# Optimization experiments

Hardware: AMD Instinct MI355X
Metric: run time of the kernel (lower is better)

The kernel has to match this reference:

```python
import jax, jax.numpy as jnp
import numpy as np
import math

B, T = 2, 1024
D_MODEL = 1024
N_HEAD = 16
HEAD_DIM = D_MODEL // N_HEAD
VOCAB = 32000
NUM_LOOP = 4
EPS_LN = 1e-5                       # torch LayerNorm default
EPS_RMS = float(np.finfo(np.float32).eps)  # torch RMSNorm eps=None -> finfo eps


def setup_inputs() -> dict:
    key = jax.random.key(0)
    ks = jax.random.split(key, 12)
    s = 0.02
    d = D_MODEL
    tok = jax.random.normal(ks[1], (VOCAB, d), jnp.float32) * s
    tok = tok.at[0].set(0.0)  # padding_idx=0
    return {
        "idx": jax.random.randint(ks[0], (B, T), 0, VOCAB),
        "tok_embed": tok,
        "ln_e_g": jnp.ones((d,), jnp.float32),
        "ln_e_b": jnp.zeros((d,), jnp.float32),
        "Wqkv": jax.random.normal(ks[2], (d, 3 * d), jnp.float32) * s,
        "bqkv": jnp.zeros((3 * d,), jnp.float32),
        "Wo": jax.random.normal(ks[3], (d, d), jnp.float32) * s,
        "bo": jnp.zeros((d,), jnp.float32),
        "W1": jax.random.normal(ks[4], (d, 4 * d), jnp.float32) * s,
        "b1": jnp.zeros((4 * d,), jnp.float32),
        "W2": jax.random.normal(ks[5], (4 * d, d), jnp.float32) * s,
        "b2": jnp.zeros((d,), jnp.float32),
        "n1_w": jnp.ones((d,), jnp.float32),
        "n2_w": jnp.ones((d,), jnp.float32),
        "lnf_g": jnp.ones((d,), jnp.float32),
        "lnf_b": jnp.zeros((d,), jnp.float32),
        "Wlm": jax.random.normal(ks[6], (d, VOCAB), jnp.float32) * s,
        "blm": jnp.zeros((VOCAB,), jnp.float32),
    }


def layernorm(x, g, b):
    m = jnp.mean(x, axis=-1, keepdims=True)
    v = jnp.mean(jnp.square(x - m), axis=-1, keepdims=True)
    return (x - m) * jax.lax.rsqrt(v + EPS_LN) * g + b


def rmsnorm(x, w):
    ms = jnp.mean(jnp.square(x), axis=-1, keepdims=True)
    return x * jax.lax.rsqrt(ms + EPS_RMS) * w


def gelu_tanh(x):
    c = math.sqrt(2.0 / math.pi)
    return 0.5 * x * (1.0 + jnp.tanh(c * (x + 0.044715 * x * x * x)))


def alibi_causal_bias(t):
    # rpe[q,k] = -(q-k) for q>k else 0, scaled per head by 2^(-8/H*(h+1)); causal -inf above diag
    pos = jnp.arange(t)
    rel = pos[:, None] - pos[None, :]                      # [T,T] = q - k
    slopes = 2.0 ** (-8.0 / N_HEAD * jnp.arange(1, N_HEAD + 1, dtype=jnp.float32))
    bias = -slopes[:, None, None] * rel.astype(jnp.float32)  # [H,T,T]
    return jnp.where(rel[None] >= 0, bias, -jnp.inf)       # causal mask fused


def reference(idx, tok_embed, ln_e_g, ln_e_b, Wqkv, bqkv, Wo, bo,
              W1, b1, W2, b2, n1_w, n2_w, lnf_g, lnf_b, Wlm, blm):
    b, t = idx.shape
    x = layernorm(tok_embed[idx], ln_e_g, ln_e_b)          # rpe=True: no sinusoidal PE
    bias = alibi_causal_bias(t)                            # [H,T,T]
    scale = 1.0 / math.sqrt(HEAD_DIM)

    for _ in range(NUM_LOOP):
        # attention sublayer
        h = rmsnorm(x, n1_w)
        qkv = h @ Wqkv + bqkv
        q, k, v = jnp.split(qkv, 3, axis=-1)
        q = q.reshape(b, t, N_HEAD, HEAD_DIM).transpose(0, 2, 1, 3)
        k = k.reshape(b, t, N_HEAD, HEAD_DIM).transpose(0, 2, 1, 3)
        v = v.reshape(b, t, N_HEAD, HEAD_DIM).transpose(0, 2, 1, 3)
        att = jnp.einsum('bhqd,bhkd->bhqk', q, k) * scale + bias[None]
        att = jax.nn.softmax(att, axis=-1)
        y = jnp.einsum('bhqk,bhkd->bhqd', att, v)
        y = y.transpose(0, 2, 1, 3).reshape(b, t, D_MODEL)
        x = x + (y @ Wo + bo)
        # mlp sublayer
        h = rmsnorm(x, n2_w)
        x = x + (gelu_tanh(h @ W1 + b1) @ W2 + b2)

    x = layernorm(x, lnf_g, lnf_b)
    return x @ Wlm + blm  # [B,T,VOCAB]
```

## Files before the change

### kernel.cpp

```cpp
#include <hip/hip_runtime.h>
#include <stdint.h>

#define DEVI __device__ __forceinline__

typedef __attribute__((ext_vector_type(8))) short short8;
typedef __attribute__((ext_vector_type(4))) float f32x4;
typedef unsigned short u16;
typedef unsigned int u32;

typedef const __attribute__((address_space(1))) void* gas_ptr;
typedef __attribute__((address_space(3))) void* las_ptr;

constexpr int BBATCH = 2;
constexpr int TT  = 1024;
constexpr int BT  = BBATCH * TT;
constexpr int DM  = 1024;
constexpr int NH  = 16;
constexpr int HD  = 64;
constexpr int DFF = 4096;
constexpr int NV  = 32000;
constexpr int NL  = 4;

DEVI u16 f2b(float f) {
  u32 u = __builtin_bit_cast(u32, f);
  u = (u + 0x7fffu + ((u >> 16) & 1u)) >> 16;
  return (u16)u;
}
DEVI float b2f(u16 h) { return __builtin_bit_cast(float, (u32)h << 16); }

DEVI void gld16(const void* g, void* l) {
  __builtin_amdgcn_global_load_lds((gas_ptr)g, (las_ptr)l, 16, 0, 0);
}

DEVI float wave_sum(float v) {
#pragma unroll
  for (int off = 32; off; off >>= 1) v += __shfl_xor(v, off);
  return v;
}
DEVI float block_sum(float v, float* sb) {
  v = wave_sum(v);
  int lane = threadIdx.x & 63, wid = threadIdx.x >> 6;
  __syncthreads();
  if (lane == 0) sb[wid] = v;
  __syncthreads();
  return sb[0] + sb[1] + sb[2] + sb[3];
}

DEVI float gelu_f(float x) {
  float u = 0.7978845608028654f * (x + 0.044715f * x * x * x);
  float e = __expf(2.0f * u);
  return x * (1.0f - 1.0f / (e + 1.0f));
}

__global__ __launch_bounds__(256) void wt_transpose_all(
    const float* __restrict__ Wqkv, const float* __restrict__ Wo,
    const float* __restrict__ W1, const float* __restrict__ W2,
    const float* __restrict__ Wlm,
    u16* __restrict__ WqkvT, u16* __restrict__ WoT, u16* __restrict__ W1T,
    u16* __restrict__ W2T, u16* __restrict__ WlmT) {
  __shared__ float t[32][33];
  int bid = blockIdx.x;
  const float* in; u16* out; int K, N, tt;
  if (bid < 3072)       { in = Wqkv; out = WqkvT; K = 1024; N = 3072;  tt = bid; }
  else if (bid < 4096)  { in = Wo;   out = WoT;   K = 1024; N = 1024;  tt = bid - 3072; }
  else if (bid < 8192)  { in = W1;   out = W1T;   K = 1024; N = 4096;  tt = bid - 4096; }
  else if (bid < 12288) { in = W2;   out = W2T;   K = 4096; N = 1024;  tt = bid - 8192; }
  else                  { in = Wlm;  out = WlmT;  K = 1024; N = 32000; tt = bid - 12288; }
  int nx = N >> 5;
  int n0 = (tt % nx) * 32, k0 = (tt / nx) * 32;
  int tx = threadIdx.x & 31, ty = threadIdx.x >> 5;
#pragma unroll
  for (int i = 0; i < 4; ++i)
    t[ty + 8 * i][tx] = in[(size_t)(k0 + ty + 8 * i) * N + n0 + tx];
  __syncthreads();
#pragma unroll
  for (int i = 0; i < 4; ++i)
    out[(size_t)(n0 + ty + 8 * i) * K + k0 + tx] = f2b(t[tx][ty + 8 * i]);
}

__global__ __launch_bounds__(256) void embed_ln_k(const int* __restrict__ idx,
                                                  const float* __restrict__ tok,
                                                  const float* __restrict__ g,
                                                  const float* __restrict__ b,
                                                  float* __restrict__ x) {
  __shared__ float sb[4];
  int row = blockIdx.x, tid = threadIdx.x;
  float4 v = ((const float4*)(tok + (size_t)idx[row] * DM))[tid];
  float s = block_sum(v.x + v.y + v.z + v.w, sb);
  float m = s * (1.0f / DM);
  float dx = v.x - m, dy = v.y - m, dz = v.z - m, dw = v.w - m;
  float q = block_sum(dx * dx + dy * dy + dz * dz + dw * dw, sb);
  float rs = rsqrtf(q * (1.0f / DM) + 1e-5f);
  float4 gg = ((const float4*)g)[tid];
  float4 bb = ((const float4*)b)[tid];
  float4 o = make_float4(dx * rs * gg.x + bb.x, dy * rs * gg.y + bb.y,
                         dz * rs * gg.z + bb.z, dw * rs * gg.w + bb.w);
  ((float4*)(x + (size_t)row * DM))[tid] = o;
}

__global__ __launch_bounds__(256) void final_ln_k(const float* __restrict__ x,
                                                  const float* __restrict__ g,
                                                  const float* __restrict__ b,
                                                  u16* __restrict__ xf) {
  __shared__ float sb[4];
  int row = blockIdx.x, tid = threadIdx.x;
  float4 v = ((const float4*)(x + (size_t)row * DM))[tid];
  float s = block_sum(v.x + v.y + v.z + v.w, sb);
  float m = s * (1.0f / DM);
  float dx = v.x - m, dy = v.y - m, dz = v.z - m, dw = v.w - m;
  float q = block_sum(dx * dx + dy * dy + dz * dz + dw * dw, sb);
  float rs = rsqrtf(q * (1.0f / DM) + 1e-5f);
  float4 gg = ((const float4*)g)[tid];
  float4 bb = ((const float4*)b)[tid];
  u32 lo = (u32)f2b(dx * rs * gg.x + bb.x) | ((u32)f2b(dy * rs * gg.y + bb.y) << 16);
  u32 hi = (u32)f2b(dz * rs * gg.z + bb.z) | ((u32)f2b(dw * rs * gg.w + bb.w) << 16);
  ((uint2*)(xf + (size_t)row * DM))[tid] = make_uint2(lo, hi);
}

__global__ __launch_bounds__(256) void rmsnorm_k(const float* __restrict__ x,
                                                 const float* __restrict__ w,
                                                 u16* __restrict__ h) {
  __shared__ float sb[4];
  int row = blockIdx.x, tid = threadIdx.x;
  float4 v = ((const float4*)(x + (size_t)row * DM))[tid];
  float q = block_sum(v.x * v.x + v.y * v.y + v.z * v.z + v.w * v.w, sb);
  float rs = rsqrtf(q * (1.0f / DM) + 1.1920928955078125e-7f);
  float4 ww = ((const float4*)w)[tid];
  u32 lo = (u32)f2b(v.x * rs * ww.x) | ((u32)f2b(v.y * rs * ww.y) << 16);
  u32 hi = (u32)f2b(v.z * rs * ww.z) | ((u32)f2b(v.w * rs * ww.w) << 16);
  ((uint2*)(h + (size_t)row * DM))[tid] = make_uint2(lo, hi);
}

__global__ __launch_bounds__(256) void attn_k(const u16* __restrict__ qkv,
                                              const u16* __restrict__ vT,
                                              u16* __restrict__ y) {
  __shared__ __align__(16) char sP[32768];
  __shared__ __align__(16) char sK[2][16384];
  __shared__ __align__(16) char sV[2][16384];
  const int tid = threadIdx.x, lane = tid & 63, wid = tid >> 6;
  const int qt = blockIdx.x, bh = blockIdx.y, b = bh >> 4, h = bh & 15;
  const float slope = exp2f(-0.5f * (float)(h + 1));

  const char* Qb = (const char*)(qkv + (size_t)b * TT * 3 * DM + h * HD);
  const char* Kb = (const char*)(qkv + (size_t)b * TT * 3 * DM + DM + h * HD);
  const char* Vb = (const char*)(vT + (size_t)bh * HD * TT);

#pragma unroll
  for (int ci = 0; ci < 4; ++ci) {
    int c = wid * 4 + ci;
    int r = c * 8 + (lane >> 3);
    int q = (lane & 7) ^ (r & 7);
    gld16(Qb + (size_t)(qt * 128 + r) * 6144 + q * 16, sP + c * 1024 + lane * 16);
  }

  auto stageKV = [&](int buf, int kt) {
    int kv0 = kt * 128;
#pragma unroll
    for (int ci = 0; ci < 4; ++ci) {
      int c = wid * 4 + ci;
      int r = c * 8 + (lane >> 3);
      int q = (lane & 7) ^ (r & 7);
      gld16(Kb + (size_t)(kv0 + r) * 6144 + q * 16, sK[buf] + c * 1024 + lane * 16);
    }
#pragma unroll
    for (int ci = 0; ci < 4; ++ci) {
      int c = wid * 4 + ci;
      int d = c * 4 + (lane >> 4);
      int q = (lane & 15) ^ (d & 15);
      gld16(Vb + (size_t)d * 2048 + (size_t)kv0 * 2 + q * 16, sV[buf] + c * 1024 + lane * 16);
    }
  };
  stageKV(0, 0);
  asm volatile("s_waitcnt vmcnt(8)" ::: "memory");

  short8 qf[2][2];
#pragma unroll
  for (int i = 0; i < 2; ++i)
#pragma unroll
    for (int ks = 0; ks < 2; ++ks) {
      int r = wid * 32 + i * 16 + (lane & 15);
      int q = ((ks << 2) + (lane >> 4)) ^ (r & 7);
      qf[i][ks] = *(const short8*)(sP + r * 128 + q * 16);
    }

  f32x4 Y[2][4] = {};
  float m_r[2][4], l_r[2][4];
#pragma unroll
  for (int i = 0; i < 2; ++i)
#pragma unroll
    for (int r = 0; r < 4; ++r) { m_r[i][r] = -3e38f; l_r[i][r] = 0.0f; }

  for (int kt = 0; kt <= qt; ++kt) {
    const int cur = kt & 1;
    if (kt < qt) {
      stageKV(cur ^ 1, kt + 1);
      asm volatile("s_waitcnt vmcnt(8)" ::: "memory");
    } else {
      asm volatile("s_waitcnt vmcnt(0)" ::: "memory");
    }
    __syncthreads();

    f32x4 s[2][8] = {};
    __builtin_amdgcn_s_setprio(1);
#pragma unroll
    for (int ks = 0; ks < 2; ++ks) {
      short8 kf[8];
#pragma unroll
      for (int j = 0; j < 8; ++j) {
        int r = j * 16 + (lane & 15);
        int q = ((ks << 2) + (lane >> 4)) ^ (r & 7);
        kf[j] = *(const short8*)(sK[cur] + r * 128 + q * 16);
      }
#pragma unroll
      for (int i = 0; i < 2; ++i)
#pragma unroll
        for (int j = 0; j < 8; ++j)
          s[i][j] = __builtin_amdgcn_mfma_f32_16x16x32_bf16(qf[i][ks], kf[j], s[i][j], 0, 0, 0);
    }
    __builtin_amdgcn_s_setprio(0);

    const int kv0 = kt * 128;
#pragma unroll
    for (int i = 0; i < 2; ++i) {
      const int qbase = qt * 128 + wid * 32 + i * 16 + ((lane >> 4) << 2);
      float rowmax[4] = {-3e38f, -3e38f, -3e38f, -3e38f};
#pragma unroll
      for (int j = 0; j < 8; ++j) {
        int kcol = kv0 + j * 16 + (lane & 15);
#pragma unroll
        for (int r = 0; r < 4; ++r) {
          int qrow = qbase + r;
          float v = (kcol <= qrow) ? s[i][j][r] * 0.125f - slope * (float)(qrow - kcol) : -3e38f;
          s[i][j][r] = v;
          rowmax[r] = fmaxf(rowmax[r], v);
        }
      }
#pragma unroll
      for (int r = 0; r < 4; ++r) {
        rowmax[r] = fmaxf(rowmax[r], __shfl_xor(rowmax[r], 1));
        rowmax[r] = fmaxf(rowmax[r], __shfl_xor(rowmax[r], 2));
        rowmax[r] = fmaxf(rowmax[r], __shfl_xor(rowmax[r], 4));
        rowmax[r] = fmaxf(rowmax[r], __shfl_xor(rowmax[r], 8));
        float mn = fmaxf(m_r[i][r], rowmax[r]);
        float al = __expf(m_r[i][r] - mn);
        m_r[i][r] = mn;
        l_r[i][r] *= al;
#pragma unroll
        for (int j = 0; j < 4; ++j) Y[i][j][r] *= al;
      }
      float rs[4] = {0.0f, 0.0f, 0.0f, 0.0f};
#pragma unroll
      for (int j = 0; j < 8; ++j)
#pragma unroll
        for (int r = 0; r < 4; ++r) {
          float p = __expf(s[i][j][r] - m_r[i][r]);
          s[i][j][r] = p;
          rs[r] += p;
        }
#pragma unroll
      for (int r = 0; r < 4; ++r) {
        rs[r] += __shfl_xor(rs[r], 1);
        rs[r] += __shfl_xor(rs[r], 2);
        rs[r] += __shfl_xor(rs[r], 4);
        rs[r] += __shfl_xor(rs[r], 8);
        l_r[i][r] += rs[r];
      }
#pragma unroll
      for (int j = 0; j < 8; ++j)
#pragma unroll
        for (int r = 0; r < 4; ++r) {
          int rl = wid * 32 + i * 16 + ((lane >> 4) << 2) + r;
          int c = j * 16 + (lane & 15);
          int g = c >> 3;
          *(u16*)(sP + rl * 256 + ((g ^ (rl & 15)) << 4) + (c & 7) * 2) = f2b(s[i][j][r]);
        }
    }

    __builtin_amdgcn_s_setprio(1);
#pragma unroll
    for (int ks = 0; ks < 4; ++ks) {
      short8 pf[2], vf[4];
#pragma unroll
      for (int i = 0; i < 2; ++i) {
        int r = wid * 32 + i * 16 + (lane & 15);
        int q = ((ks << 2) + (lane >> 4)) ^ (r & 15);
        pf[i] = *(const short8*)(sP + r * 256 + (q << 4));
      }
#pragma unroll
      for (int j = 0; j < 4; ++j) {
        int d = j * 16 + (lane & 15);
        int q = ((ks << 2) + (lane >> 4)) ^ (d & 15);
        vf[j] = *(const short8*)(sV[cur] + d * 256 + (q << 4));
      }
#pragma unroll
      for (int i = 0; i < 2; ++i)
#pragma unroll
        for (int j = 0; j < 4; ++j)
          Y[i][j] = __builtin_amdgcn_mfma_f32_16x16x32_bf16(pf[i], vf[j], Y[i][j], 0, 0, 0);
    }
    __builtin_amdgcn_s_setprio(0);
    __syncthreads();
  }

#pragma unroll
  for (int i = 0; i < 2; ++i)
#pragma unroll
    for (int r = 0; r < 4; ++r) {
      float inv = 1.0f / l_r[i][r];
      int qrow = qt * 128 + wid * 32 + i * 16 + ((lane >> 4) << 2) + r;
      u16* yp = y + (size_t)(b * TT + qrow) * DM + h * HD;
#pragma unroll
      for (int j = 0; j < 4; ++j)
        yp[j * 16 + (lane & 15)] = f2b(Y[i][j][r] * inv);
    }
}

enum { EPI_BF16 = 0, EPI_GELU = 1, EPI_ADDF32 = 2, EPI_F32 = 3, EPI_ATOMIC = 4, EPI_QKV = 5 };

template <int BM, int BN, int WM, int WN, int EPI, int KS = 1>
__global__ __launch_bounds__(256, 2) void gemm_bt(
    const u16* __restrict__ A, int lda, const u16* __restrict__ Bt, int ldb,
    const float* __restrict__ bias, void* __restrict__ C, int ldc,
    float* __restrict__ resid, int K, u16* __restrict__ vTout) {
  constexpr int BK = 64;
  constexpr int NW = WM * WN;
  constexpr int FM = BM / WM / 16, FN = BN / WN / 16;
  constexpr int ABYTES = BM * BK * 2, BBYTES = BN * BK * 2;
  constexpr int ACH = ABYTES / 1024, BCH = BBYTES / 1024, NCH = ACH + BCH;
  extern __shared__ __align__(16) char smem[];

  const int tid = threadIdx.x, lane = tid & 63, wid = tid >> 6;
  const int brow = blockIdx.y * BM, bcol = blockIdx.x * BN;
  const long long kbase2 = (long long)blockIdx.z * (K / KS) * 2;

  const int nt = (K / KS) >> 6;
  const int widm = wid / WN, widn = wid % WN;
  const int rm0 = widm * (BM / WM), cn0 = widn * (BN / WN);

  f32x4 acc[FM][FN] = {};

  const int swq16 = (((lane & 7) ^ ((lane >> 3) & 7)) << 4);
  const int lrow8 = lane >> 3;

  auto stage = [&](int buf, int kt) {
    char* base = smem + buf * (ABYTES + BBYTES);
    const char* Ag = (const char*)A;
    const char* Bg = (const char*)Bt;
    long long kOff = kbase2 + (long long)kt * 128 + swq16;
#pragma unroll
    for (int ci = 0; ci < NCH / NW; ++ci) {
      int c = wid + ci * NW;
      if (c < ACH) {
        int r = c * 8 + lrow8;
        gld16(Ag + (long long)(brow + r) * (lda * 2) + kOff, base + c * 1024 + lane * 16);
      } else {
        int r = (c - ACH) * 8 + lrow8;
        gld16(Bg + (long long)(bcol + r) * (ldb * 2) + kOff,
              base + ABYTES + (c - ACH) * 1024 + lane * 16);
      }
    }
  };

  auto compute = [&](int buf) {
    char* baseA = smem + buf * (ABYTES + BBYTES);
    char* baseB = baseA + ABYTES;
#pragma unroll
    for (int ks = 0; ks < 2; ++ks) {
      short8 af[FM], bv[FN];
#pragma unroll
      for (int i = 0; i < FM; ++i) {
        int r = rm0 + i * 16 + (lane & 15);
        int cq = ((ks << 2) + (lane >> 4)) ^ (r & 7);
        af[i] = *(const short8*)(baseA + r * 128 + (cq << 4));
      }
#pragma unroll
      for (int j = 0; j < FN; ++j) {
        int r = cn0 + j * 16 + (lane & 15);
        int cq = ((ks << 2) + (lane >> 4)) ^ (r & 7);
        bv[j] = *(const short8*)(baseB + r * 128 + (cq << 4));
      }
#pragma unroll
      for (int i = 0; i < FM; ++i)
#pragma unroll
        for (int j = 0; j < FN; ++j)
          acc[i][j] = __builtin_amdgcn_mfma_f32_16x16x32_bf16(af[i], bv[j], acc[i][j], 0, 0, 0);
    }
  };

  stage(0, 0);
  __syncthreads();
  int cur = 0;
  for (int t = 0; t < nt; ++t) {
    if (t + 1 < nt) stage(cur ^ 1, t + 1);
    compute(cur);
    __syncthreads();
    cur ^= 1;
  }

  if constexpr (EPI == EPI_QKV) {
    if (bcol >= 2 * DM) {
      u16* st = (u16*)smem;
#pragma unroll
      for (int i = 0; i < FM; ++i)
#pragma unroll
        for (int j = 0; j < FN; ++j)
#pragma unroll
          for (int r = 0; r < 4; ++r) {
            int rl = rm0 + i * 16 + ((lane >> 4) << 2) + r;
            int cl = cn0 + j * 16 + (lane & 15);
            st[rl * 130 + cl] = f2b(acc[i][j][r] + bias[bcol + cl]);
          }
      __syncthreads();
      const int b = brow >> 10, t0b = brow & (TT - 1);
      const int h0 = (bcol - 2 * DM) >> 6;
      const int sub = tid & 15;
#pragma unroll
      for (int pass = 0; pass < 8; ++pass) {
        int d = pass * 16 + (tid >> 4);
        u32 pk[4];
#pragma unroll
        for (int k2 = 0; k2 < 4; ++k2) {
          u16 lo = st[(sub * 8 + 2 * k2) * 130 + d];
          u16 hi = st[(sub * 8 + 2 * k2 + 1) * 130 + d];
          pk[k2] = (u32)lo | ((u32)hi << 16);
        }
        int head = h0 + (d >> 6), dd = d & 63;
        *(uint4*)(vTout + ((size_t)((b * NH + head) * HD + dd)) * TT + t0b + sub * 8) =
            make_uint4(pk[0], pk[1], pk[2], pk[3]);
      }
      return;
    }
  }

  const int r0 = brow + rm0 + ((lane >> 4) << 2);
  const int c0 = bcol + cn0 + (lane & 15);
#pragma unroll
  for (int i = 0; i < FM; ++i) {
#pragma unroll
    for (int j = 0; j < FN; ++j) {
#pragma unroll
      for (int r = 0; r < 4; ++r) {
        int row = r0 + i * 16 + r;
        int col = c0 + j * 16;
        float v = acc[i][j][r];
        if constexpr (EPI == EPI_BF16 || EPI == EPI_QKV) {
          ((u16*)C)[(size_t)row * ldc + col] = f2b(v + bias[col]);
        } else if constexpr (EPI == EPI_GELU) {
          ((u16*)C)[(size_t)row * ldc + col] = f2b(gelu_f(v + bias[col]));
        } else if constexpr (EPI == EPI_ADDF32) {
          size_t o = (size_t)row * ldc + col;
          resid[o] += v + bias[col];
        } else if constexpr (EPI == EPI_ATOMIC) {
          size_t o = (size_t)row * ldc + col;
          atomicAdd(&resid[o], v + (blockIdx.z == 0 ? bias[col] : 0.0f));
        } else {
          ((float*)C)[(size_t)row * ldc + col] = v + bias[col];
        }
      }
    }
  }
}

template <int EPI>
__global__ __launch_bounds__(512, 2) void gemm8(
    const u16* __restrict__ A, int lda, const u16* __restrict__ Bt, int ldb,
    const float* __restrict__ bias, void* __restrict__ C, int ldc, int K, int nby) {
  __shared__ __align__(16) char smem[2][2][32768];
  const int tid = threadIdx.x, lane = tid & 63;
  const int wid = tid >> 6, wm = wid >> 2, wn = wid & 3;

  const int nb = gridDim.x;
  const int q8 = nb >> 3, r8 = nb & 7;
  const int xcd = blockIdx.x & 7, lin = blockIdx.x >> 3;
  const int idx = (xcd < r8 ? xcd * (q8 + 1) : r8 * (q8 + 1) + (xcd - r8) * q8) + lin;
  const int brow = (idx % nby) * 256, bcol = (idx / nby) * 256;

  const int nt = K >> 6, niter = nt >> 1;

  const int srow = tid >> 3, sq = tid & 7;
  auto stage = [&](int buf, int isB, int half, int kt) {
    const u16* G = isB ? Bt : A;
    const int ld = isB ? ldb : lda;
    const int base = isB ? bcol : brow;
    char* L = &smem[buf][isB][half * 16384];
#pragma unroll
    for (int l = 0; l < 2; ++l) {
      int rl = half * 128 + l * 64 + srow;
      gld16((const char*)G + (size_t)(base + rl) * (ld * 2) + kt * 128 + ((sq ^ (rl & 7)) << 4),
            L + l * 8192 + tid * 16);
    }
  };

  short8 bfr[4][2], afr[2][2];
  f32x4 acc[8][4] = {};

  stage(0, 0, 0, 0); stage(0, 0, 1, 0);
  stage(0, 1, 0, 0); stage(0, 1, 1, 0);
  stage(1, 1, 0, 1); stage(1, 1, 1, 1);
  asm volatile("s_waitcnt vmcnt(0)" ::: "memory");
  __builtin_amdgcn_s_barrier();

  for (int i = 0; i < niter; ++i) {
    const bool full = (i + 1 < niter);
    const int t2 = 2 * i + 2, t3 = 2 * i + 3;
#pragma unroll
    for (int h = 0; h < 2; ++h) {
#pragma unroll
      for (int qd = 0; qd < 4; ++qd) {
        if (qd == 0) {
#pragma unroll
          for (int j = 0; j < 4; ++j)
#pragma unroll
            for (int ks = 0; ks < 2; ++ks) {
              int r = wn * 64 + j * 16 + (lane & 15);
              int q = ((ks << 2) + (lane >> 4)) ^ (r & 7);
              bfr[j][ks] = *(const short8*)&smem[h][1][r * 128 + q * 16];
            }
        }
#pragma unroll
        for (int f = 0; f < 2; ++f)
#pragma unroll
          for (int ks = 0; ks < 2; ++ks) {
            int r = wm * 128 + (qd * 2 + f) * 16 + (lane & 15);
            int q = ((ks << 2) + (lane >> 4)) ^ (r & 7);
            afr[f][ks] = *(const short8*)&smem[h][0][r * 128 + q * 16];
          }
        if (h == 0) {
          if (qd == 0) stage(1, 0, 0, 2 * i + 1);
          else if (qd == 1) stage(1, 0, 1, 2 * i + 1);
          else if (qd == 2) { if (full) stage(0, 1, 0, t2); }
          else              { if (full) stage(0, 1, 1, t2); }
        } else {
          if (qd == 0)      { if (full) stage(0, 0, 0, t2); }
          else if (qd == 1) { if (full) stage(0, 0, 1, t2); }
          else if (qd == 2) { if (full) stage(1, 1, 0, t3); }
          else              { if (full) stage(1, 1, 1, t3); }
        }
        if (qd == 3) {
          if (full) asm volatile("s_waitcnt vmcnt(4)" ::: "memory");
          else if (h == 0) asm volatile("s_waitcnt vmcnt(0)" ::: "memory");
        }
        __builtin_amdgcn_s_barrier();
        asm volatile("s_waitcnt lgkmcnt(0)" ::: "memory");
        __builtin_amdgcn_s_setprio(1);
#pragma unroll
        for (int f = 0; f < 2; ++f)
#pragma unroll
          for (int j = 0; j < 4; ++j)
#pragma unroll
            for (int ks = 0; ks < 2; ++ks)
              acc[qd * 2 + f][j] = __builtin_amdgcn_mfma_f32_16x16x32_bf16(
                  afr[f][ks], bfr[j][ks], acc[qd * 2 + f][j], 0, 0, 0);
        __builtin_amdgcn_s_setprio(0);
        __builtin_amdgcn_s_barrier();
      }
    }
  }

  const int r0 = brow + wm * 128 + ((lane >> 4) << 2);
  const int c0 = bcol + wn * 64 + (lane & 15);
#pragma unroll
  for (int fi = 0; fi < 8; ++fi) {
#pragma unroll
    for (int j = 0; j < 4; ++j) {
      int col = c0 + j * 16;
      float bv = bias[col];
#pragma unroll
      for (int r = 0; r < 4; ++r) {
        int row = r0 + fi * 16 + r;
        float v = acc[fi][j][r] + bv;
        if constexpr (EPI == EPI_F32)
          ((float*)C)[(size_t)row * ldc + col] = v;
        else if constexpr (EPI == EPI_GELU)
          ((u16*)C)[(size_t)row * ldc + col] = f2b(gelu_f(v));
        else
          ((u16*)C)[(size_t)row * ldc + col] = f2b(v);
      }
    }
  }
}

extern "C" void kernel_launch(void* const* d_in, const int* in_sizes, int n_in,
                              void* d_out, int out_size, void* d_ws, size_t ws_size,
                              hipStream_t stream) {
  (void)in_sizes; (void)n_in; (void)out_size;
  const int*   idx    = (const int*)d_in[0];
  const float* tok    = (const float*)d_in[1];
  const float* ln_e_g = (const float*)d_in[2];
  const float* ln_e_b = (const float*)d_in[3];
  const float* Wqkv   = (const float*)d_in[4];
  const float* bqkv   = (const float*)d_in[5];
  const float* Wo     = (const float*)d_in[6];
  const float* bo     = (const float*)d_in[7];
  const float* W1     = (const float*)d_in[8];
  const float* b1     = (const float*)d_in[9];
  const float* W2     = (const float*)d_in[10];
  const float* b2     = (const float*)d_in[11];
  const float* n1_w   = (const float*)d_in[12];
  const float* n2_w   = (const float*)d_in[13];
  const float* lnf_g  = (const float*)d_in[14];
  const float* lnf_b  = (const float*)d_in[15];
  const float* Wlm    = (const float*)d_in[16];
  const float* blm    = (const float*)d_in[17];
  float* out = (float*)d_out;

  char* w = (char*)d_ws;
  auto alloc = [&](size_t bytes) { char* p = w; w += (bytes + 255) & ~(size_t)255; return p; };
  float* x   = (float*)alloc((size_t)BT * DM * 4);
  u16* h     = (u16*)alloc((size_t)BT * DM * 2);
  u16* qkv   = (u16*)alloc((size_t)BT * 3 * DM * 2);
  u16* vT    = (u16*)alloc((size_t)BBATCH * NH * HD * TT * 2);
  u16* y     = (u16*)alloc((size_t)BT * DM * 2);
  u16* act   = (u16*)alloc((size_t)BT * DFF * 2);
  u16* xf    = (u16*)alloc((size_t)BT * DM * 2);
  u16* WqkvT = (u16*)alloc((size_t)3 * DM * DM * 2);
  u16* WoT   = (u16*)alloc((size_t)DM * DM * 2);
  u16* W1T   = (u16*)alloc((size_t)DFF * DM * 2);
  u16* W2T   = (u16*)alloc((size_t)DM * DFF * 2);
  u16* WlmT  = (u16*)alloc((size_t)NV * DM * 2);
  if ((size_t)(w - (char*)d_ws) > ws_size) return;

  wt_transpose_all<<<44288, 256, 0, stream>>>(Wqkv, Wo, W1, W2, Wlm,
                                              WqkvT, WoT, W1T, W2T, WlmT);

  embed_ln_k<<<BT, 256, 0, stream>>>(idx, tok, ln_e_g, ln_e_b, x);

  constexpr int SM128 = 2 * (128 * 64 * 2 + 128 * 64 * 2);
  constexpr int SM64  = 2 * (128 * 64 * 2 + 64 * 64 * 2);

  for (int l = 0; l < NL; ++l) {
    rmsnorm_k<<<BT, 256, 0, stream>>>(x, n1_w, h);
    gemm_bt<128, 128, 2, 2, EPI_QKV><<<dim3(3 * DM / 128, BT / 128), 256, SM128, stream>>>(
        h, DM, WqkvT, DM, bqkv, qkv, 3 * DM, nullptr, DM, vT);
    attn_k<<<dim3(TT / 128, BBATCH * NH), 256, 0, stream>>>(qkv, vT, y);
    gemm_bt<128, 64, 4, 1, EPI_ATOMIC, 2><<<dim3(DM / 64, BT / 128, 2), 256, SM64, stream>>>(
        y, DM, WoT, DM, bo, nullptr, DM, x, DM, nullptr);
    rmsnorm_k<<<BT, 256, 0, stream>>>(x, n2_w, h);
    gemm_bt<128, 128, 2, 2, EPI_GELU><<<dim3(DFF / 128, BT / 128), 256, SM128, stream>>>(
        h, DM, W1T, DM, b1, act, DFF, nullptr, DM, nullptr);
    gemm_bt<128, 128, 2, 2, EPI_ATOMIC, 4><<<dim3(DM / 128, BT / 128, 4), 256, SM128, stream>>>(
        act, DFF, W2T, DFF, b2, nullptr, DM, x, DFF, nullptr);
  }

  final_ln_k<<<BT, 256, 0, stream>>>(x, lnf_g, lnf_b, xf);
  gemm8<EPI_F32><<<dim3((NV / 256) * (BT / 256)), 512, 0, stream>>>(
      xf, DM, WlmT, DM, blm, out, NV, DM, BT / 256);
}
```

Before: 906.0 us.

## Split attention into 64-row query tiles with balanced ordering; stage LM-head stores via LDS

Attention now processes 64-row query tiles over a flat 512-block grid. Block indices are remapped so that long and short causal tiles interleave, and the KV double buffer is dropped to cut LDS use and raise occupancy. The fp32 LM-head GEMM epilogue writes its accumulators through swizzled shared memory and then emits coalesced float4 row stores. The trade-off is losing the KV load/compute overlap in attention and adding extra barriers in the epilogue.

Measured after the change: 851.5 us. -6.0%, faster.

```diff
diff --git a/kernel.cpp b/kernel.cpp
--- a/kernel.cpp
+++ b/kernel.cpp
@@ -134,11 +134,15 @@
 __global__ __launch_bounds__(256) void attn_k(const u16* __restrict__ qkv,
                                               const u16* __restrict__ vT,
                                               u16* __restrict__ y) {
-  __shared__ __align__(16) char sP[32768];
-  __shared__ __align__(16) char sK[2][16384];
-  __shared__ __align__(16) char sV[2][16384];
+  __shared__ __align__(16) char sP[16384];
+  __shared__ __align__(16) char sK[16384];
+  __shared__ __align__(16) char sV[16384];
   const int tid = threadIdx.x, lane = tid & 63, wid = tid >> 6;
-  const int qt = blockIdx.x, bh = blockIdx.y, b = bh >> 4, h = bh & 15;
+  const int bid = blockIdx.x;
+  const int sl = (bid + (bid >> 8)) & 15;
+  const int qt = (sl & 1) ? (sl >> 1) : (15 - (sl >> 1));
+  const int bh = (bid >> 4) & 31, b = bh >> 4, h = bh & 15;
+  const int nt = (qt >> 1) + 1;
   const float slope = exp2f(-0.5f * (float)(h + 1));
 
   const char* Qb = (const char*)(qkv + (size_t)b * TT * 3 * DM + h * HD);
@@ -146,61 +150,51 @@
   const char* Vb = (const char*)(vT + (size_t)bh * HD * TT);
 
 #pragma unroll
-  for (int ci = 0; ci < 4; ++ci) {
-    int c = wid * 4 + ci;
+  for (int ci = 0; ci < 2; ++ci) {
+    int c = wid * 2 + ci;
     int r = c * 8 + (lane >> 3);
     int q = (lane & 7) ^ (r & 7);
-    gld16(Qb + (size_t)(qt * 128 + r) * 6144 + q * 16, sP + c * 1024 + lane * 16);
-  }
-
-  auto stageKV = [&](int buf, int kt) {
+    gld16(Qb + (size_t)(qt * 64 + r) * 6144 + q * 16, sP + c * 1024 + lane * 16);
+  }
+
+  auto stageKV = [&](int kt) {
     int kv0 = kt * 128;
 #pragma unroll
     for (int ci = 0; ci < 4; ++ci) {
       int c = wid * 4 + ci;
       int r = c * 8 + (lane >> 3);
       int q = (lane & 7) ^ (r & 7);
-      gld16(Kb + (size_t)(kv0 + r) * 6144 + q * 16, sK[buf] + c * 1024 + lane * 16);
+      gld16(Kb + (size_t)(kv0 + r) * 6144 + q * 16, sK + c * 1024 + lane * 16);
     }
 #pragma unroll
     for (int ci = 0; ci < 4; ++ci) {
       int c = wid * 4 + ci;
       int d = c * 4 + (lane >> 4);
       int q = (lane & 15) ^ (d & 15);
-      gld16(Vb + (size_t)d * 2048 + (size_t)kv0 * 2 + q * 16, sV[buf] + c * 1024 + lane * 16);
+      gld16(Vb + (size_t)d * 2048 + (size_t)kv0 * 2 + q * 16, sV + c * 1024 + lane * 16);
     }
   };
-  stageKV(0, 0);
+  stageKV(0);
   asm volatile("s_waitcnt vmcnt(8)" ::: "memory");
 
-  short8 qf[2][2];
-#pragma unroll
-  for (int i = 0; i < 2; ++i)
-#pragma unroll
-    for (int ks = 0; ks < 2; ++ks) {
-      int r = wid * 32 + i * 16 + (lane & 15);
-      int q = ((ks << 2) + (lane >> 4)) ^ (r & 7);
-      qf[i][ks] = *(const short8*)(sP + r * 128 + q * 16);
-    }
-
-  f32x4 Y[2][4] = {};
-  float m_r[2][4], l_r[2][4];
-#pragma unroll
-  for (int i = 0; i < 2; ++i)
-#pragma unroll
-    for (int r = 0; r < 4; ++r) { m_r[i][r] = -3e38f; l_r[i][r] = 0.0f; }
-
-  for (int kt = 0; kt <= qt; ++kt) {
-    const int cur = kt & 1;
-    if (kt < qt) {
-      stageKV(cur ^ 1, kt + 1);
-      asm volatile("s_waitcnt vmcnt(8)" ::: "memory");
-    } else {
-      asm volatile("s_waitcnt vmcnt(0)" ::: "memory");
-    }
+  short8 qf[2];
+#pragma unroll
+  for (int ks = 0; ks < 2; ++ks) {
+    int r = wid * 16 + (lane & 15);
+    int q = ((ks << 2) + (lane >> 4)) ^ (r & 7);
+    qf[ks] = *(const short8*)(sP + r * 128 + q * 16);
+  }
+
+  f32x4 Y[4] = {};
+  float m_r[4], l_r[4];
+#pragma unroll
+  for (int r = 0; r < 4; ++r) { m_r[r] = -3e38f; l_r[r] = 0.0f; }
+
+  for (int kt = 0; kt < nt; ++kt) {
+    asm volatile("s_waitcnt vmcnt(0)" ::: "memory");
     __syncthreads();
 
-    f32x4 s[2][8] = {};
+    f32x4 s[8] = {};
     __builtin_amdgcn_s_setprio(1);
 #pragma unroll
     for (int ks = 0; ks < 2; ++ks) {
@@ -209,110 +203,101 @@
       for (int j = 0; j < 8; ++j) {
         int r = j * 16 + (lane & 15);
         int q = ((ks << 2) + (lane >> 4)) ^ (r & 7);
-        kf[j] = *(const short8*)(sK[cur] + r * 128 + q * 16);
-      }
-#pragma unroll
-      for (int i = 0; i < 2; ++i)
-#pragma unroll
-        for (int j = 0; j < 8; ++j)
-          s[i][j] = __builtin_amdgcn_mfma_f32_16x16x32_bf16(qf[i][ks], kf[j], s[i][j], 0, 0, 0);
+        kf[j] = *(const short8*)(sK + r * 128 + q * 16);
+      }
+#pragma unroll
+      for (int j = 0; j < 8; ++j)
+        s[j] = __builtin_amdgcn_mfma_f32_16x16x32_bf16(qf[ks], kf[j], s[j], 0, 0, 0);
     }
     __builtin_amdgcn_s_setprio(0);
 
     const int kv0 = kt * 128;
-#pragma unroll
-    for (int i = 0; i < 2; ++i) {
-      const int qbase = qt * 128 + wid * 32 + i * 16 + ((lane >> 4) << 2);
-      float rowmax[4] = {-3e38f, -3e38f, -3e38f, -3e38f};
-#pragma unroll
-      for (int j = 0; j < 8; ++j) {
-        int kcol = kv0 + j * 16 + (lane & 15);
-#pragma unroll
-        for (int r = 0; r < 4; ++r) {
-          int qrow = qbase + r;
-          float v = (kcol <= qrow) ? s[i][j][r] * 0.125f - slope * (float)(qrow - kcol) : -3e38f;
-          s[i][j][r] = v;
-          rowmax[r] = fmaxf(rowmax[r], v);
-        }
-      }
+    const int qbase = qt * 64 + wid * 16 + ((lane >> 4) << 2);
+    float rowmax[4] = {-3e38f, -3e38f, -3e38f, -3e38f};
+#pragma unroll
+    for (int j = 0; j < 8; ++j) {
+      int kcol = kv0 + j * 16 + (lane & 15);
 #pragma unroll
       for (int r = 0; r < 4; ++r) {
-        rowmax[r] = fmaxf(rowmax[r], __shfl_xor(rowmax[r], 1));
-        rowmax[r] = fmaxf(rowmax[r], __shfl_xor(rowmax[r], 2));
-        rowmax[r] = fmaxf(rowmax[r], __shfl_xor(rowmax[r], 4));
-        rowmax[r] = fmaxf(rowmax[r], __shfl_xor(rowmax[r], 8));
-        float mn = fmaxf(m_r[i][r], rowmax[r]);
-        float al = __expf(m_r[i][r] - mn);
-        m_r[i][r] = mn;
-        l_r[i][r] *= al;
-#pragma unroll
-        for (int j = 0; j < 4; ++j) Y[i][j][r] *= al;
-      }
-      float rs[4] = {0.0f, 0.0f, 0.0f, 0.0f};
-#pragma unroll
-      for (int j = 0; j < 8; ++j)
-#pragma unroll
-        for (int r = 0; r < 4; ++r) {
-          float p = __expf(s[i][j][r] - m_r[i][r]);
-          s[i][j][r] = p;
-          rs[r] += p;
-        }
+        int qrow = qbase + r;
+        float v = (kcol <= qrow) ? s[j][r] * 0.125f - slope * (float)(qrow - kcol) : -3e38f;
+        s[j][r] = v;
+        rowmax[r] = fmaxf(rowmax[r], v);
+      }
+    }
+#pragma unroll
+    for (int r = 0; r < 4; ++r) {
+      rowmax[r] = fmaxf(rowmax[r], __shfl_xor(rowmax[r], 1));
+      rowmax[r] = fmaxf(rowmax[r], __shfl_xor(rowmax[r], 2));
+      rowmax[r] = fmaxf(rowmax[r], __shfl_xor(rowmax[r], 4));
+      rowmax[r] = fmaxf(rowmax[r], __shfl_xor(rowmax[r], 8));
+      float mn = fmaxf(m_r[r], rowmax[r]);
+      float al = __expf(m_r[r] - mn);
+      m_r[r] = mn;
+      l_r[r] *= al;
+#pragma unroll
+      for (int j = 0; j < 4; ++j) Y[j][r] *= al;
+    }
+    float rs[4] = {0.0f, 0.0f, 0.0f, 0.0f};
+#pragma unroll
+    for (int j = 0; j < 8; ++j)
 #pragma unroll
       for (int r = 0; r < 4; ++r) {
-        rs[r] += __shfl_xor(rs[r], 1);
-        rs[r] += __shfl_xor(rs[r], 2);
-        rs[r] += __shfl_xor(rs[r], 4);
-        rs[r] += __shfl_xor(rs[r], 8);
-        l_r[i][r] += rs[r];
-      }
-#pragma unroll
-      for (int j = 0; j < 8; ++j)
-#pragma unroll
-        for (int r = 0; r < 4; ++r) {
-          int rl = wid * 32 + i * 16 + ((lane >> 4) << 2) + r;
-          int c = j * 16 + (lane & 15);
-          int g = c >> 3;
-          *(u16*)(sP + rl * 256 + ((g ^ (rl & 15)) << 4) + (c & 7) * 2) = f2b(s[i][j][r]);
-        }
-    }
+        float p = __expf(s[j][r] - m_r[r]);
+        s[j][r] = p;
+        rs[r] += p;
+      }
+#pragma unroll
+    for (int r = 0; r < 4; ++r) {
+      rs[r] += __shfl_xor(rs[r], 1);
+      rs[r] += __shfl_xor(rs[r], 2);
+      rs[r] += __shfl_xor(rs[r], 4);
+      rs[r] += __shfl_xor(rs[r], 8);
+      l_r[r] += rs[r];
+    }
+#pragma unroll
+    for (int j = 0; j < 8; ++j)
+#pragma unroll
+      for (int r = 0; r < 4; ++r) {
+        int rl = wid * 16 + ((lane >> 4) << 2) + r;
+        int c = j * 16 + (lane & 15);
+        int g = c >> 3;
+        *(u16*)(sP + rl * 256 + ((g ^ (rl & 15)) << 4) + (c & 7) * 2) = f2b(s[j][r]);
+      }
 
     __builtin_amdgcn_s_setprio(1);
 #pragma unroll
     for (int ks = 0; ks < 4; ++ks) {
-      short8 pf[2], vf[4];
-#pragma unroll
-      for (int i = 0; i < 2; ++i) {
-        int r = wid * 32 + i * 16 + (lane & 15);
+      short8 pf, vf[4];
+      {
+        int r = wid * 16 + (lane & 15);
         int q = ((ks << 2) + (lane >> 4)) ^ (r & 15);
-        pf[i] = *(const short8*)(sP + r * 256 + (q << 4));
+        pf = *(const short8*)(sP + r * 256 + (q << 4));
       }
 #pragma unroll
       for (int j = 0; j < 4; ++j) {
         int d = j * 16 + (lane & 15);
         int q = ((ks << 2) + (lane >> 4)) ^ (d & 15);
-        vf[j] = *(const short8*)(sV[cur] + d * 256 + (q << 4));
-      }
-#pragma unroll
-      for (int i = 0; i < 2; ++i)
-#pragma unroll
-        for (int j = 0; j < 4; ++j)
-          Y[i][j] = __builtin_amdgcn_mfma_f32_16x16x32_bf16(pf[i], vf[j], Y[i][j], 0, 0, 0);
+        vf[j] = *(const short8*)(sV + d * 256 + (q << 4));
+      }
+#pragma unroll
+      for (int j = 0; j < 4; ++j)
+        Y[j] = __builtin_amdgcn_mfma_f32_16x16x32_bf16(pf, vf[j], Y[j], 0, 0, 0);
     }
     __builtin_amdgcn_s_setprio(0);
     __syncthreads();
-  }
-
-#pragma unroll
-  for (int i = 0; i < 2; ++i)
-#pragma unroll
-    for (int r = 0; r < 4; ++r) {
-      float inv = 1.0f / l_r[i][r];
-      int qrow = qt * 128 + wid * 32 + i * 16 + ((lane >> 4) << 2) + r;
-      u16* yp = y + (size_t)(b * TT + qrow) * DM + h * HD;
-#pragma unroll
-      for (int j = 0; j < 4; ++j)
-        yp[j * 16 + (lane & 15)] = f2b(Y[i][j][r] * inv);
-    }
+    if (kt + 1 < nt) stageKV(kt + 1);
+  }
+
+#pragma unroll
+  for (int r = 0; r < 4; ++r) {
+    float inv = 1.0f / l_r[r];
+    int qrow = qt * 64 + wid * 16 + ((lane >> 4) << 2) + r;
+    u16* yp = y + (size_t)(b * TT + qrow) * DM + h * HD;
+#pragma unroll
+    for (int j = 0; j < 4; ++j)
+      yp[j * 16 + (lane & 15)] = f2b(Y[j][r] * inv);
+  }
 }
 
 enum { EPI_BF16 = 0, EPI_GELU = 1, EPI_ADDF32 = 2, EPI_F32 = 3, EPI_ATOMIC = 4, EPI_QKV = 5 };
@@ -557,6 +542,39 @@
     }
   }
 
+  if constexpr (EPI == EPI_F32) {
+    char* sf = &smem[0][0][0];
+    float* C32 = (float*)C;
+#pragma unroll
+    for (int half = 0; half < 2; ++half) {
+      if (wm == half) {
+#pragma unroll
+        for (int fi = 0; fi < 8; ++fi)
+#pragma unroll
+          for (int j = 0; j < 4; ++j) {
+            int cl = wn * 64 + j * 16 + (lane & 15);
+            float bv = bias[bcol + cl];
+            int qsw = (cl >> 2);
+#pragma unroll
+            for (int r = 0; r < 4; ++r) {
+              int row = fi * 16 + ((lane >> 4) << 2) + r;
+              *(float*)(sf + row * 1024 + ((qsw ^ (row & 7)) << 4) + (cl & 3) * 4) =
+                  acc[fi][j][r] + bv;
+            }
+          }
+      }
+      __syncthreads();
+#pragma unroll
+      for (int pass = 0; pass < 16; ++pass) {
+        int row = pass * 8 + wid;
+        float4 v4 = *(float4*)(sf + row * 1024 + ((lane ^ (row & 7)) << 4));
+        *(float4*)(C32 + (size_t)(brow + half * 128 + row) * ldc + bcol + lane * 4) = v4;
+      }
+      __syncthreads();
+    }
+    return;
+  }
+
   const int r0 = brow + wm * 128 + ((lane >> 4) << 2);
   const int c0 = bcol + wn * 64 + (lane & 15);
 #pragma unroll
@@ -569,9 +587,7 @@
       for (int r = 0; r < 4; ++r) {
         int row = r0 + fi * 16 + r;
         float v = acc[fi][j][r] + bv;
-        if constexpr (EPI == EPI_F32)
-          ((float*)C)[(size_t)row * ldc + col] = v;
-        else if constexpr (EPI == EPI_GELU)
+        if constexpr (EPI == EPI_GELU)
           ((u16*)C)[(size_t)row * ldc + col] = f2b(gelu_f(v));
         else
           ((u16*)C)[(size_t)row * ldc + col] = f2b(v);
@@ -632,7 +648,7 @@
     rmsnorm_k<<<BT, 256, 0, stream>>>(x, n1_w, h);
     gemm_bt<128, 128, 2, 2, EPI_QKV><<<dim3(3 * DM / 128, BT / 128), 256, SM128, stream>>>(
         h, DM, WqkvT, DM, bqkv, qkv, 3 * DM, nullptr, DM, vT);
-    attn_k<<<dim3(TT / 128, BBATCH * NH), 256, 0, stream>>>(qkv, vT, y);
+    attn_k<<<512, 256, 0, stream>>>(qkv, vT, y);
     gemm_bt<128, 64, 4, 1, EPI_ATOMIC, 2><<<dim3(DM / 64, BT / 128, 2), 256, SM64, stream>>>(
         y, DM, WoT, DM, bo, nullptr, DM, x, DM, nullptr);
     rmsnorm_k<<<BT, 256, 0, stream>>>(x, n2_w, h);
```
